# Optimization experiments

Hardware: AMD Instinct MI355X
Metric: run time of the kernel (lower is better)

The kernel has to match this reference:

```python
import jax, jax.numpy as jnp
import numpy as np

N = 100000      # nodes
E = 800000      # edges (avg degree 8)
F = 61          # num_node_features (embedding dim); node feat = F+3 = 64 with pos
D = 64          # hidden_dim
OUT = 32        # output_dim
TYPES = 100     # num_node_types
G = 64          # number of graphs in the batch (global_mean_pool segments)
L = 4           # num_layers per SE3Transformer (from transformer_config)


def _mk(k, shape):
    return jax.random.normal(k, shape, jnp.float32) * 0.1


def setup_inputs() -> dict:
    key = jax.random.key(0)
    ks = jax.random.split(key, 24)
    din = F + 3  # cat([pos, embedding(z)])
    inp = {
        "pos": jax.random.normal(ks[0], (N, 3), jnp.float32),
        "z": jax.random.randint(ks[1], (N,), 0, TYPES),
        "edge_index": jax.random.randint(ks[2], (2, E), 0, N),
        "batch": jnp.sort(jax.random.randint(ks[3], (N,), 0, G)),
        "emb": _mk(ks[4], (TYPES, F)),
        # transformer1: input proj din->D, then L message-passing layers at width D
        "t1_Win": _mk(ks[5], (din, D)),
        "t1_W1": _mk(ks[6], (L, 2 * D + 1, D)), "t1_b1": jnp.zeros((L, D), jnp.float32),
        "t1_W2": _mk(ks[7], (L, D, D)),        "t1_b2": jnp.zeros((L, D), jnp.float32),
        "t1_W3": _mk(ks[8], (L, 2 * D, D)),    "t1_b3": jnp.zeros((L, D), jnp.float32),
        # transformer2: input proj D->D, then L layers at width D
        "t2_Win": _mk(ks[9], (D, D)),
        "t2_W1": _mk(ks[10], (L, 2 * D + 1, D)), "t2_b1": jnp.zeros((L, D), jnp.float32),
        "t2_W2": _mk(ks[11], (L, D, D)),         "t2_b2": jnp.zeros((L, D), jnp.float32),
        "t2_W3": _mk(ks[12], (L, 2 * D, D)),     "t2_b3": jnp.zeros((L, D), jnp.float32),
        # final Linear(hidden_dim, output_dim)
        "Wlin": _mk(ks[13], (D, OUT)), "blin": jnp.zeros((OUT,), jnp.float32),
    }
    return inp


def _transformer(h, pos, src, dst, Win, W1, b1, W2, b2, W3, b3):
    """Equivariant graph transformer block: input projection + L distance-
    conditioned message-passing layers with residual updates."""
    h = h @ Win  # [N, D]
    # squared pairwise distance per edge -> rotation/translation invariant
    d2 = jnp.sum((pos[src] - pos[dst]) ** 2, axis=-1, keepdims=True)  # [E, 1]

    def layer(h, p):
        W1, b1, W2, b2, W3, b3 = p
        m = jnp.concatenate([h[src], h[dst], d2], axis=-1)        # [E, 2D+1]
        m = jax.nn.relu(m @ W1 + b1) @ W2 + b2                    # [E, D]
        agg = jax.ops.segment_sum(m, dst, num_segments=N)          # [N, D]
        h = h + jax.nn.relu(jnp.concatenate([h, agg], axis=-1) @ W3 + b3)
        return h, None

    h, _ = jax.lax.scan(layer, h, (W1, b1, W2, b2, W3, b3))
    return h


def reference(pos, z, edge_index, batch, emb,
              t1_Win, t1_W1, t1_b1, t1_W2, t1_b2, t1_W3, t1_b3,
              t2_Win, t2_W1, t2_b1, t2_W2, t2_b2, t2_W3, t2_b3,
              Wlin, blin):
    src, dst = edge_index[0], edge_index[1]
    x = jnp.concatenate([pos, emb[z]], axis=-1)  # [N, 3+F]
    x = jax.nn.relu(_transformer(x, pos, src, dst, t1_Win, t1_W1, t1_b1, t1_W2, t1_b2, t1_W3, t1_b3))
    x = jax.nn.relu(_transformer(x, pos, src, dst, t2_Win, t2_W1, t2_b1, t2_W2, t2_b2, t2_W3, t2_b3))
    x = x @ Wlin + blin  # [N, OUT]
    # global_mean_pool over graph ids
    counts = jax.ops.segment_sum(jnp.ones((N,), x.dtype), batch, num_segments=G)
    pooled = jax.ops.segment_sum(x, batch, num_segments=G) / jnp.clip(counts, 1.0)[:, None]
    return pooled  # [G, OUT]
```

## Files before the change

### kernel.cpp

```cpp
#include <hip/hip_runtime.h>
#include <hip/hip_bf16.h>

typedef unsigned short u16;
typedef unsigned int   u32;
typedef short bf16x8 __attribute__((ext_vector_type(8)));
typedef float f32x4  __attribute__((ext_vector_type(4)));

#define NN 100000
#define EE 800000
#define NTILE 6250
#define NTB   1563
#define EBLK  1792
#define TOTW  (EBLK * 4)
#define SCB   98
#define GMAX  (NN + EE / 8 + 2)

#define MFMA16(a,b,c) __builtin_amdgcn_mfma_f32_16x16x32_bf16(a,b,c,0,0,0)

__device__ __forceinline__ float b2f(u16 u) {
    u32 x = ((u32)u) << 16;
    return __uint_as_float(x);
}
__device__ __forceinline__ u16 f2b(float f) {
    __hip_bfloat16 h = __float2bfloat16(f);
    return *reinterpret_cast<u16*>(&h);
}
__device__ __forceinline__ void splt(float v, u16& hi, u16& lo) {
    hi = f2b(v);
    lo = f2b(v - b2f(hi));
}

__global__ __launch_bounds__(256) void k_deg(const int* __restrict__ dst,
                                             int* __restrict__ deg) {
    int e = blockIdx.x * 256 + threadIdx.x;
    if (e < EE) atomicAdd(&deg[dst[e]], 1);
}

__global__ __launch_bounds__(1024) void k_scanA(const int* __restrict__ deg,
                                                int* __restrict__ part) {
    __shared__ int s[1024];
    int i = blockIdx.x * 1024 + threadIdx.x;
    int v = (i < NN) ? deg[i] : 0;
    s[threadIdx.x] = v;
    __syncthreads();
    for (int off = 512; off > 0; off >>= 1) {
        if ((int)threadIdx.x < off) s[threadIdx.x] += s[threadIdx.x + off];
        __syncthreads();
    }
    if (threadIdx.x == 0) part[blockIdx.x] = s[0];
}

__global__ void k_scanB(int* __restrict__ part) {
    if (threadIdx.x == 0 && blockIdx.x == 0) {
        int run = 0;
        for (int b = 0; b < SCB; ++b) { int v = part[b]; part[b] = run; run += v; }
        part[SCB] = run;
    }
}

__global__ __launch_bounds__(1024) void k_scanC(const int* __restrict__ deg,
                                                const int* __restrict__ part,
                                                int* __restrict__ rowptr) {
    __shared__ int s[1024];
    int i = blockIdx.x * 1024 + threadIdx.x;
    int v = (i < NN) ? deg[i] : 0;
    s[threadIdx.x] = v;
    __syncthreads();
    for (int off = 1; off < 1024; off <<= 1) {
        int t = ((int)threadIdx.x >= off) ? s[threadIdx.x - off] : 0;
        __syncthreads();
        s[threadIdx.x] += t;
        __syncthreads();
    }
    int incl = s[threadIdx.x];
    if (i < NN) rowptr[i] = part[blockIdx.x] + incl - v;
    if (i == NN - 1) rowptr[NN] = part[SCB];
}

__global__ __launch_bounds__(256) void k_scatter(const int* __restrict__ src,
                                                 const int* __restrict__ dst,
                                                 const float* __restrict__ pos,
                                                 int* __restrict__ cursor,
                                                 int* __restrict__ srcc,
                                                 float* __restrict__ d2c) {
    int e = blockIdx.x * 256 + threadIdx.x;
    if (e >= EE) return;
    if (e < 16) { srcc[EE + e] = 0; d2c[EE + e] = 0.f; }
    int d = dst[e], s = src[e];
    int p = atomicAdd(&cursor[d], 1);
    srcc[p] = s;
    float dx = pos[s * 3 + 0] - pos[d * 3 + 0];
    float dy = pos[s * 3 + 1] - pos[d * 3 + 1];
    float dz = pos[s * 3 + 2] - pos[d * 3 + 2];
    d2c[p] = dx * dx + dy * dy + dz * dz;
}

__global__ __launch_bounds__(256) void k_ngrp(const int* __restrict__ deg,
                                              int* __restrict__ ngrp) {
    int i = blockIdx.x * 256 + threadIdx.x;
    if (i < NN) ngrp[i] = (deg[i] + 7) >> 3;
}

__global__ __launch_bounds__(256) void k_gfill(const int* __restrict__ deg,
                                               const int* __restrict__ rowptr,
                                               const int* __restrict__ grp_ptr,
                                               int* __restrict__ gnode,
                                               int* __restrict__ gstart,
                                               int* __restrict__ gcnt) {
    int n = blockIdx.x * 256 + threadIdx.x;
    if (n >= NN) return;
    int d = deg[n];
    int ng = (d + 7) >> 3;
    int base = grp_ptr[n], rp = rowptr[n];
    for (int k = 0; k < ng; ++k) {
        gnode[base + k] = n;
        gstart[base + k] = rp + 8 * k;
        int cc = d - 8 * k; if (cc > 8) cc = 8;
        gcnt[base + k] = cc;
    }
}

__global__ __launch_bounds__(256) void k_swz(const float* t1W1, const float* t1W2, const float* t1W3,
                                             const float* t2W1, const float* t2W2, const float* t2W3,
                                             const float* t1Win, const float* t2Win,
                                             u16* __restrict__ WsA, u16* __restrict__ WsB) {
    int gid = blockIdx.x * 256 + threadIdx.x;
    if (gid < 163840) {
        int L = gid / 20480;
        int r = gid % 20480;
        const float* W1 = (L < 4 ? t1W1 : t2W1) + (size_t)(L & 3) * 129 * 64;
        const float* W2 = (L < 4 ? t1W2 : t2W2) + (size_t)(L & 3) * 64 * 64;
        const float* W3 = (L < 4 ? t1W3 : t2W3) + (size_t)(L & 3) * 128 * 64;
        float w;
        int rr, f, e, lane, j, row, col;
        if (r < 8192) { rr = r; f = rr >> 9; e = rr & 511; lane = e >> 3; j = e & 7;
            row = (f >> 2) * 32 + (lane >> 4) * 8 + j; col = (f & 3) * 16 + (lane & 15);
            w = W1[row * 64 + col];
        } else if (r < 12288) { rr = r - 8192; f = rr >> 9; e = rr & 511; lane = e >> 3; j = e & 7;
            row = (f >> 2) * 32 + (lane >> 4) * 8 + j; col = (f & 3) * 16 + (lane & 15);
            w = W2[row * 64 + col];
        } else { rr = r - 12288; f = rr >> 9; e = rr & 511; lane = e >> 3; j = e & 7;
            row = (f >> 2) * 32 + (lane >> 4) * 8 + j; col = (f & 3) * 16 + (lane & 15);
            w = W3[row * 64 + col];
        }
        u16 hi, lo; splt(w, hi, lo);
        WsA[(size_t)L * 40960 + r] = hi;
        WsA[(size_t)L * 40960 + 20480 + r] = lo;
    } else {
        int t = gid - 163840;
        int sel = (t < 4096) ? 0 : 1;
        int rr = t & 4095;
        const float* Win = sel ? t2Win : t1Win;
        int f = rr >> 9, e = rr & 511, lane = e >> 3, j = e & 7;
        int row = (f >> 2) * 32 + (lane >> 4) * 8 + j;
        int col = (f & 3) * 16 + (lane & 15);
        float w = Win[row * 64 + col];
        u16 hi, lo; splt(w, hi, lo);
        WsB[sel * 8192 + rr] = hi;
        WsB[sel * 8192 + 4096 + rr] = lo;
    }
}

__global__ __launch_bounds__(256) void k_proj1(const float* __restrict__ pos,
                                               const int* __restrict__ z,
                                               const float* __restrict__ emb,
                                               const u16* __restrict__ WinS,
                                               u16* __restrict__ hbx) {
    int tile = blockIdx.x * 4 + (threadIdx.x >> 6);
    if (tile >= NTILE) return;
    int lane = threadIdx.x & 63, c = lane & 15, g = lane >> 4;
    int n0 = tile * 16, nr = n0 + c;
    int zr = z[nr];
    const float* er = emb + (long)zr * 61 - 3;
    bf16x8 A0h, A0l, A1h, A1l;
#pragma unroll
    for (int j = 0; j < 8; ++j) {
        int f = 8 * g + j;
        float v1 = (f < 3) ? pos[nr * 3 + (f < 3 ? f : 0)] : er[f];
        float v2 = er[32 + 8 * g + j];
        u16 hi, lo;
        splt(v1, hi, lo); A0h[j] = (short)hi; A0l[j] = (short)lo;
        splt(v2, hi, lo); A1h[j] = (short)hi; A1l[j] = (short)lo;
    }
    const bf16x8* Wh = (const bf16x8*)WinS;
    const bf16x8* Wl = (const bf16x8*)(WinS + 4096);
#pragma unroll
    for (int nt = 0; nt < 4; ++nt) {
        f32x4 acc = {0.f, 0.f, 0.f, 0.f};
        acc = MFMA16(A0h, Wh[nt * 64 + lane], acc);
        acc = MFMA16(A1h, Wh[(4 + nt) * 64 + lane], acc);
        acc = MFMA16(A0l, Wh[nt * 64 + lane], acc);
        acc = MFMA16(A1l, Wh[(4 + nt) * 64 + lane], acc);
        acc = MFMA16(A0h, Wl[nt * 64 + lane], acc);
        acc = MFMA16(A1h, Wl[(4 + nt) * 64 + lane], acc);
#pragma unroll
        for (int r = 0; r < 4; ++r) {
            long n = n0 + 4 * g + r;
            u16 hi, lo; splt(acc[r], hi, lo);
            hbx[n * 128 + nt * 16 + c] = hi;
            hbx[n * 128 + 64 + nt * 16 + c] = lo;
        }
    }
}

__global__ __launch_bounds__(256) void k_proj2(const u16* __restrict__ WinS,
                                               u16* __restrict__ hbx) {
    int tile = blockIdx.x * 4 + (threadIdx.x >> 6);
    if (tile >= NTILE) return;
    int lane = threadIdx.x & 63, c = lane & 15, g = lane >> 4;
    int n0 = tile * 16, nr = n0 + c;
    const bf16x8* p = (const bf16x8*)(hbx + (long)nr * 128);
    bf16x8 h0 = p[g], h1 = p[g + 4], l0 = p[g + 8], l1 = p[g + 12];
    bf16x8 A0h, A0l, A1h, A1l;
#pragma unroll
    for (int j = 0; j < 8; ++j) {
        float v1 = fmaxf(b2f((u16)h0[j]) + b2f((u16)l0[j]), 0.f);
        float v2 = fmaxf(b2f((u16)h1[j]) + b2f((u16)l1[j]), 0.f);
        u16 hi, lo;
        splt(v1, hi, lo); A0h[j] = (short)hi; A0l[j] = (short)lo;
        splt(v2, hi, lo); A1h[j] = (short)hi; A1l[j] = (short)lo;
    }
    const bf16x8* Wh = (const bf16x8*)WinS;
    const bf16x8* Wl = (const bf16x8*)(WinS + 4096);
#pragma unroll
    for (int nt = 0; nt < 4; ++nt) {
        f32x4 acc = {0.f, 0.f, 0.f, 0.f};
        acc = MFMA16(A0h, Wh[nt * 64 + lane], acc);
        acc = MFMA16(A1h, Wh[(4 + nt) * 64 + lane], acc);
        acc = MFMA16(A0l, Wh[nt * 64 + lane], acc);
        acc = MFMA16(A1l, Wh[(4 + nt) * 64 + lane], acc);
        acc = MFMA16(A0h, Wl[nt * 64 + lane], acc);
        acc = MFMA16(A1h, Wl[(4 + nt) * 64 + lane], acc);
#pragma unroll
        for (int r = 0; r < 4; ++r) {
            long n = n0 + 4 * g + r;
            u16 hi, lo; splt(acc[r], hi, lo);
            hbx[n * 128 + nt * 16 + c] = hi;
            hbx[n * 128 + 64 + nt * 16 + c] = lo;
        }
    }
}

__global__ __launch_bounds__(256) void k_dsthalf(const u16* __restrict__ hbx,
                                                 const u16* __restrict__ Wsl,
                                                 const float* __restrict__ b1,
                                                 float* __restrict__ accbT) {
    int tile = blockIdx.x * 4 + (threadIdx.x >> 6);
    if (tile >= NTILE) return;
    int lane = threadIdx.x & 63, c = lane & 15, g = lane >> 4;
    int n0 = tile * 16, nr = n0 + c;
    const bf16x8* W1h = (const bf16x8*)Wsl;
    const bf16x8* W1l = (const bf16x8*)(Wsl + 20480);
    const bf16x8* p = (const bf16x8*)(hbx + (long)nr * 128);
    bf16x8 A0h = p[g], A1h = p[g + 4], A0l = p[g + 8], A1l = p[g + 12];
    f32x4 acc4[4];
#pragma unroll
    for (int nt = 0; nt < 4; ++nt) {
        float bv = b1[nt * 16 + c];
        f32x4 acc = {bv, bv, bv, bv};
        acc = MFMA16(A0h, W1h[(8 + nt) * 64 + lane], acc);
        acc = MFMA16(A1h, W1h[(12 + nt) * 64 + lane], acc);
        acc = MFMA16(A0l, W1h[(8 + nt) * 64 + lane], acc);
        acc = MFMA16(A1l, W1h[(12 + nt) * 64 + lane], acc);
        acc = MFMA16(A0h, W1l[(8 + nt) * 64 + lane], acc);
        acc = MFMA16(A1h, W1l[(12 + nt) * 64 + lane], acc);
        acc4[nt] = acc;
    }
#pragma unroll
    for (int r = 0; r < 4; ++r) {
        f32x4 w = {acc4[0][r], acc4[1][r], acc4[2][r], acc4[3][r]};
        *(f32x4*)(accbT + (long)(n0 + 4 * g + r) * 64 + c * 4) = w;
    }
}

__global__ __launch_bounds__(256) void k_edges_mfma(const u16* __restrict__ hbx,
                                                    float* __restrict__ sgrp,
                                                    const float* __restrict__ d2c,
                                                    const int* __restrict__ srcc,
                                                    const int* __restrict__ gnode,
                                                    const int* __restrict__ gstart,
                                                    const int* __restrict__ gcnt,
                                                    const int* __restrict__ grp_ptr,
                                                    const u16* __restrict__ Wsl,
                                                    const float* __restrict__ W1f,
                                                    const float* __restrict__ accbT) {
    int lane = threadIdx.x & 63;
    int wid = blockIdx.x * 4 + (threadIdx.x >> 6);
    int c = lane & 15, g = lane >> 4;
    const bf16x8* W1H = (const bf16x8*)Wsl;
    const bf16x8* W1L = (const bf16x8*)(Wsl + 20480);
    bf16x8 w1h[2][4], w1l[2][4];
#pragma unroll
    for (int ks = 0; ks < 2; ++ks)
#pragma unroll
        for (int nt = 0; nt < 4; ++nt) {
            w1h[ks][nt] = W1H[(ks * 4 + nt) * 64 + lane];
            w1l[ks][nt] = W1L[(ks * 4 + nt) * 64 + lane];
        }
    float wdc[4];
#pragma unroll
    for (int nt = 0; nt < 4; ++nt) wdc[nt] = W1f[128 * 64 + nt * 16 + c];

    int G = grp_ptr[NN];
    int T = (G + 1) >> 1;

    for (int ti = wid; ti < T; ti += TOTW) {
        int ga = 2 * ti, gb = 2 * ti + 1;
        int na = gnode[ga], sa = gstart[ga], ca = gcnt[ga];
        int nb = na, sb = sa, cb = 0;
        if (gb < G) { nb = gnode[gb]; sb = gstart[gb]; cb = gcnt[gb]; }

        int nsel = (g < 2) ? na : nb;
        int ssel = (g < 2) ? sa : sb;
        int csel = (g < 2) ? ca : cb;
        int ro = 4 * (g & 1);

        f32x4 bse = *(const f32x4*)(accbT + (long)nsel * 64 + c * 4);

        int t = (c < 8) ? (sa + c) : (sb + c - 8);
        int s = srcc[t];
        const bf16x8* sp = (const bf16x8*)(hbx + (long)s * 128);
        bf16x8 A0h = sp[g], A1h = sp[g + 4], A0l = sp[g + 8], A1l = sp[g + 12];

        float dq[4];
#pragma unroll
        for (int r = 0; r < 4; ++r) dq[r] = d2c[ssel + ro + r];

        float sv[4];
#pragma unroll
        for (int nt = 0; nt < 4; ++nt) {
            f32x4 ci;
#pragma unroll
            for (int r = 0; r < 4; ++r) ci[r] = bse[nt] + dq[r] * wdc[nt];
            ci = MFMA16(A0h, w1h[0][nt], ci);
            ci = MFMA16(A1h, w1h[1][nt], ci);
            ci = MFMA16(A0l, w1h[0][nt], ci);
            ci = MFMA16(A1l, w1h[1][nt], ci);
            ci = MFMA16(A0h, w1l[0][nt], ci);
            ci = MFMA16(A1h, w1l[1][nt], ci);
            float s4 = 0.f;
#pragma unroll
            for (int r = 0; r < 4; ++r)
                s4 += (ro + r < csel) ? fmaxf(ci[r], 0.f) : 0.f;
            s4 += __shfl_xor(s4, 16);
            sv[nt] = s4;
        }
        if (g == 0) {
#pragma unroll
            for (int nt = 0; nt < 4; ++nt)
                sgrp[(long)ga * 64 + nt * 16 + c] = sv[nt];
        }
        if (g == 2 && gb < G) {
#pragma unroll
            for (int nt = 0; nt < 4; ++nt)
                sgrp[(long)gb * 64 + nt * 16 + c] = sv[nt];
        }
    }
}

__global__ __launch_bounds__(256) void k_node2(u16* __restrict__ hbx,
                                               const float* __restrict__ sgrp,
                                               const int* __restrict__ grp_ptr,
                                               const int* __restrict__ deg,
                                               const u16* __restrict__ Wsl,
                                               const float* __restrict__ b2,
                                               const float* __restrict__ b3,
                                               const u16* __restrict__ WslN,
                                               const float* __restrict__ b1N,
                                               float* __restrict__ accbT) {
    __shared__ u16 th[4][16 * 72];
    __shared__ u16 tl[4][16 * 72];
    int w = threadIdx.x >> 6, lane = threadIdx.x & 63;
    int tile = blockIdx.x * 4 + w;
    if (tile >= NTILE) return;
    int c = lane & 15, g = lane >> 4;
    int n0 = tile * 16, nr = n0 + c;
    u16* lh = th[w];
    u16* ll = tl[w];

    const bf16x8* W2H = (const bf16x8*)(Wsl + 8192);
    const bf16x8* W2L = (const bf16x8*)(Wsl + 28672);
    const bf16x8* W3H = (const bf16x8*)(Wsl + 12288);
    const bf16x8* W3L = (const bf16x8*)(Wsl + 32768);

    int gp0 = grp_ptr[nr], gp1 = grp_ptr[nr + 1];
    f32x4 sA0 = {0, 0, 0, 0}, sA1 = {0, 0, 0, 0};
    f32x4 sB0 = {0, 0, 0, 0}, sB1 = {0, 0, 0, 0};
    for (int gi = gp0; gi < gp1; ++gi) {
        const f32x4* q = (const f32x4*)(sgrp + (long)gi * 64 + 8 * g);
        const f32x4* q2 = (const f32x4*)(sgrp + (long)gi * 64 + 32 + 8 * g);
        sA0 += q[0]; sA1 += q[1];
        sB0 += q2[0]; sB1 += q2[1];
    }
    bf16x8 S0h, S0l, S1h, S1l;
#pragma unroll
    for (int j = 0; j < 4; ++j) {
        u16 hi, lo;
        splt(sA0[j], hi, lo); S0h[j] = (short)hi; S0l[j] = (short)lo;
        splt(sA1[j], hi, lo); S0h[4 + j] = (short)hi; S0l[4 + j] = (short)lo;
        splt(sB0[j], hi, lo); S1h[j] = (short)hi; S1l[j] = (short)lo;
        splt(sB1[j], hi, lo); S1h[4 + j] = (short)hi; S1l[4 + j] = (short)lo;
    }

    const bf16x8* hp = (const bf16x8*)(hbx + (long)nr * 128);
    bf16x8 H0h = hp[g], H1h = hp[g + 4], H0l = hp[g + 8], H1l = hp[g + 12];

    float dg[4];
#pragma unroll
    for (int r = 0; r < 4; ++r) dg[r] = (float)deg[n0 + 4 * g + r];

#pragma unroll
    for (int nt = 0; nt < 4; ++nt) {
        float b2c = b2[nt * 16 + c];
        f32x4 a = {dg[0] * b2c, dg[1] * b2c, dg[2] * b2c, dg[3] * b2c};
        a = MFMA16(S0h, W2H[nt * 64 + lane], a);
        a = MFMA16(S1h, W2H[(4 + nt) * 64 + lane], a);
        a = MFMA16(S0l, W2H[nt * 64 + lane], a);
        a = MFMA16(S1l, W2H[(4 + nt) * 64 + lane], a);
        a = MFMA16(S0h, W2L[nt * 64 + lane], a);
        a = MFMA16(S1h, W2L[(4 + nt) * 64 + lane], a);
#pragma unroll
        for (int r = 0; r < 4; ++r) {
            u16 hi, lo; splt(a[r], hi, lo);
            lh[(4 * g + r) * 72 + nt * 16 + c] = hi;
            ll[(4 * g + r) * 72 + nt * 16 + c] = lo;
        }
    }
    bf16x8 G0h = *(const bf16x8*)(lh + c * 72 + g * 8);
    bf16x8 G1h = *(const bf16x8*)(lh + c * 72 + 32 + g * 8);
    bf16x8 G0l = *(const bf16x8*)(ll + c * 72 + g * 8);
    bf16x8 G1l = *(const bf16x8*)(ll + c * 72 + 32 + g * 8);

    f32x4 u4[4];
#pragma unroll
    for (int nt = 0; nt < 4; ++nt) {
        float bv = b3[nt * 16 + c];
        f32x4 u = {bv, bv, bv, bv};
        u = MFMA16(H0h, W3H[nt * 64 + lane], u);
        u = MFMA16(H1h, W3H[(4 + nt) * 64 + lane], u);
        u = MFMA16(G0h, W3H[(8 + nt) * 64 + lane], u);
        u = MFMA16(G1h, W3H[(12 + nt) * 64 + lane], u);
        u = MFMA16(H0l, W3H[nt * 64 + lane], u);
        u = MFMA16(H1l, W3H[(4 + nt) * 64 + lane], u);
        u = MFMA16(G0l, W3H[(8 + nt) * 64 + lane], u);
        u = MFMA16(G1l, W3H[(12 + nt) * 64 + lane], u);
        u = MFMA16(H0h, W3L[nt * 64 + lane], u);
        u = MFMA16(H1h, W3L[(4 + nt) * 64 + lane], u);
        u = MFMA16(G0h, W3L[(8 + nt) * 64 + lane], u);
        u = MFMA16(G1h, W3L[(12 + nt) * 64 + lane], u);
        u4[nt] = u;
    }

#pragma unroll
    for (int nt = 0; nt < 4; ++nt)
#pragma unroll
        for (int r = 0; r < 4; ++r) {
            long n = n0 + 4 * g + r;
            long ix = n * 128 + nt * 16 + c;
            float ho = b2f(hbx[ix]) + b2f(hbx[ix + 64]);
            float hn = ho + fmaxf(u4[nt][r], 0.f);
            u16 hi, lo; splt(hn, hi, lo);
            hbx[ix] = hi;
            hbx[ix + 64] = lo;
            lh[(4 * g + r) * 72 + nt * 16 + c] = hi;
            ll[(4 * g + r) * 72 + nt * 16 + c] = lo;
        }

    if (WslN) {
        bf16x8 N0h = *(const bf16x8*)(lh + c * 72 + g * 8);
        bf16x8 N1h = *(const bf16x8*)(lh + c * 72 + 32 + g * 8);
        bf16x8 N0l = *(const bf16x8*)(ll + c * 72 + g * 8);
        bf16x8 N1l = *(const bf16x8*)(ll + c * 72 + 32 + g * 8);
        const bf16x8* W1h = (const bf16x8*)WslN;
        const bf16x8* W1l = (const bf16x8*)(WslN + 20480);
        f32x4 acc4[4];
#pragma unroll
        for (int nt = 0; nt < 4; ++nt) {
            float bv = b1N[nt * 16 + c];
            f32x4 a = {bv, bv, bv, bv};
            a = MFMA16(N0h, W1h[(8 + nt) * 64 + lane], a);
            a = MFMA16(N1h, W1h[(12 + nt) * 64 + lane], a);
            a = MFMA16(N0l, W1h[(8 + nt) * 64 + lane], a);
            a = MFMA16(N1l, W1h[(12 + nt) * 64 + lane], a);
            a = MFMA16(N0h, W1l[(8 + nt) * 64 + lane], a);
            a = MFMA16(N1h, W1l[(12 + nt) * 64 + lane], a);
            acc4[nt] = a;
        }
#pragma unroll
        for (int r = 0; r < 4; ++r) {
            f32x4 wv = {acc4[0][r], acc4[1][r], acc4[2][r], acc4[3][r]};
            *(f32x4*)(accbT + (long)(n0 + 4 * g + r) * 64 + c * 4) = wv;
        }
    }
}

__global__ void k_granges(const int* __restrict__ batch, int* __restrict__ gpt) {
    int g = blockIdx.x * blockDim.x + threadIdx.x;
    if (g > 64) return;
    int lo = 0, hi = NN;
    while (lo < hi) {
        int mid = (lo + hi) >> 1;
        if (batch[mid] < g) lo = mid + 1; else hi = mid;
    }
    gpt[g] = lo;
}

__global__ __launch_bounds__(256) void k_sumrelu(const u16* __restrict__ hbx,
                                                 const int* __restrict__ gpt,
                                                 float* __restrict__ sumh) {
    int g = blockIdx.x >> 3, sp = blockIdx.x & 7;
    int lo = gpt[g], hi = gpt[g + 1];
    int n = hi - lo;
    int per = (n + 7) / 8;
    int s0 = lo + sp * per;
    int s1 = s0 + per; if (s1 > hi) s1 = hi;
    int lane = threadIdx.x & 63, wv = threadIdx.x >> 6;
    float acc = 0.f;
    for (int i = s0 + wv; i < s1; i += 4) {
        float v = b2f(hbx[(long)i * 128 + lane]) + b2f(hbx[(long)i * 128 + 64 + lane]);
        acc += fmaxf(v, 0.f);
    }
    if (acc != 0.f || wv == 0)
        atomicAdd(&sumh[g * 64 + lane], acc);
}

__global__ __launch_bounds__(256) void k_outgemm(const float* __restrict__ sumh,
                                                 const int* __restrict__ gpt,
                                                 const float* __restrict__ Wlin,
                                                 const float* __restrict__ blin,
                                                 float* __restrict__ out) {
    int idx = blockIdx.x * 256 + threadIdx.x;
    if (idx >= 64 * 32) return;
    int g = idx >> 5, o = idx & 31;
    int cnt = gpt[g + 1] - gpt[g];
    float acc = 0.f;
#pragma unroll 8
    for (int k = 0; k < 64; ++k)
        acc += sumh[g * 64 + k] * Wlin[k * 32 + o];
    out[idx] = (cnt > 0) ? (acc / (float)cnt + blin[o]) : 0.f;
}

extern "C" void kernel_launch(void* const* d_in, const int* in_sizes, int n_in,
                              void* d_out, int out_size, void* d_ws, size_t ws_size,
                              hipStream_t stream) {
    const float* pos    = (const float*)d_in[0];
    const int*   z      = (const int*)d_in[1];
    const int*   ei     = (const int*)d_in[2];
    const int*   batch  = (const int*)d_in[3];
    const float* emb    = (const float*)d_in[4];
    const float* t1_Win = (const float*)d_in[5];
    const float* t1_W1  = (const float*)d_in[6];
    const float* t1_b1  = (const float*)d_in[7];
    const float* t1_W2  = (const float*)d_in[8];
    const float* t1_b2  = (const float*)d_in[9];
    const float* t1_W3  = (const float*)d_in[10];
    const float* t1_b3  = (const float*)d_in[11];
    const float* t2_Win = (const float*)d_in[12];
    const float* t2_W1  = (const float*)d_in[13];
    const float* t2_b1  = (const float*)d_in[14];
    const float* t2_W2  = (const float*)d_in[15];
    const float* t2_b2  = (const float*)d_in[16];
    const float* t2_W3  = (const float*)d_in[17];
    const float* t2_b3  = (const float*)d_in[18];
    const float* Wlin   = (const float*)d_in[19];
    const float* blin   = (const float*)d_in[20];

    const int* srcI = ei;
    const int* dstI = ei + EE;

    char* ws = (char*)d_ws;
    size_t off = 0;
    auto alloc = [&](size_t bytes) -> void* {
        void* p = ws + off;
        off += (bytes + 255) / 256 * 256;
        return p;
    };
    float* accbT   = (float*)alloc((size_t)NN * 64 * 4);
    u16*   hbx     = (u16*)alloc((size_t)NN * 128 * 2);
    float* sgrp    = (float*)alloc((size_t)GMAX * 64 * 4);
    int*   rowptr  = (int*)alloc((size_t)(NN + 1) * 4);
    int*   deg     = (int*)alloc((size_t)NN * 4);
    int*   cursor  = (int*)alloc((size_t)NN * 4);
    int*   ngrpA   = (int*)alloc((size_t)NN * 4);
    int*   grp_ptr = (int*)alloc((size_t)(NN + 1) * 4);
    int*   gnode   = (int*)alloc((size_t)GMAX * 4);
    int*   gstart  = (int*)alloc((size_t)GMAX * 4);
    int*   gcnt    = (int*)alloc((size_t)GMAX * 4);
    int*   srcc    = (int*)alloc((size_t)(EE + 16) * 4);
    float* d2c     = (float*)alloc((size_t)(EE + 16) * 4);
    int*   gpt     = (int*)alloc(65 * 4);
    float* sumh    = (float*)alloc(64 * 64 * 4);
    int*   part    = (int*)alloc((SCB + 1) * 4);
    u16*   WsA     = (u16*)alloc((size_t)8 * 40960 * 2);
    u16*   WsB     = (u16*)alloc((size_t)16384 * 2);

    hipMemsetAsync(deg, 0, (size_t)NN * 4, stream);
    k_deg<<<(EE + 255) / 256, 256, 0, stream>>>(dstI, deg);
    k_scanA<<<SCB, 1024, 0, stream>>>(deg, part);
    k_scanB<<<1, 64, 0, stream>>>(part);
    k_scanC<<<SCB, 1024, 0, stream>>>(deg, part, rowptr);
    hipMemcpyAsync(cursor, rowptr, (size_t)NN * 4, hipMemcpyDeviceToDevice, stream);
    k_scatter<<<(EE + 255) / 256, 256, 0, stream>>>(srcI, dstI, pos, cursor, srcc, d2c);
    k_ngrp<<<(NN + 255) / 256, 256, 0, stream>>>(deg, ngrpA);
    k_scanA<<<SCB, 1024, 0, stream>>>(ngrpA, part);
    k_scanB<<<1, 64, 0, stream>>>(part);
    k_scanC<<<SCB, 1024, 0, stream>>>(ngrpA, part, grp_ptr);
    k_gfill<<<(NN + 255) / 256, 256, 0, stream>>>(deg, rowptr, grp_ptr, gnode, gstart, gcnt);
    k_swz<<<172032 / 256, 256, 0, stream>>>(t1_W1, t1_W2, t1_W3, t2_W1, t2_W2, t2_W3,
                                            t1_Win, t2_Win, WsA, WsB);
    k_granges<<<1, 128, 0, stream>>>(batch, gpt);

    k_proj1<<<NTB, 256, 0, stream>>>(pos, z, emb, WsB, hbx);
    k_dsthalf<<<NTB, 256, 0, stream>>>(hbx, WsA, t1_b1, accbT);
    for (int l = 0; l < 4; ++l) {
        const u16* Wsl = WsA + (size_t)l * 40960;
        k_edges_mfma<<<EBLK, 256, 0, stream>>>(hbx, sgrp, d2c, srcc, gnode, gstart,
                                               gcnt, grp_ptr, Wsl,
                                               t1_W1 + (size_t)l * 129 * 64, accbT);
        const u16* WslN = (l < 3) ? (WsA + (size_t)(l + 1) * 40960) : nullptr;
        const float* b1N = (l < 3) ? (t1_b1 + (size_t)(l + 1) * 64) : nullptr;
        k_node2<<<NTB, 256, 0, stream>>>(hbx, sgrp, grp_ptr, deg, Wsl,
                                         t1_b2 + (size_t)l * 64, t1_b3 + (size_t)l * 64,
                                         WslN, b1N, accbT);
    }

    k_proj2<<<NTB, 256, 0, stream>>>(WsB + 8192, hbx);
    k_dsthalf<<<NTB, 256, 0, stream>>>(hbx, WsA + (size_t)4 * 40960, t2_b1, accbT);
    for (int l = 0; l < 4; ++l) {
        const u16* Wsl = WsA + (size_t)(4 + l) * 40960;
        k_edges_mfma<<<EBLK, 256, 0, stream>>>(hbx, sgrp, d2c, srcc, gnode, gstart,
                                               gcnt, grp_ptr, Wsl,
                                               t2_W1 + (size_t)l * 129 * 64, accbT);
        const u16* WslN = (l < 3) ? (WsA + (size_t)(5 + l) * 40960) : nullptr;
        const float* b1N = (l < 3) ? (t2_b1 + (size_t)(l + 1) * 64) : nullptr;
        k_node2<<<NTB, 256, 0, stream>>>(hbx, sgrp, grp_ptr, deg, Wsl,
                                         t2_b2 + (size_t)l * 64, t2_b3 + (size_t)l * 64,
                                         WslN, b1N, accbT);
    }

    hipMemsetAsync(sumh, 0, 64 * 64 * 4, stream);
    k_sumrelu<<<64 * 8, 256, 0, stream>>>(hbx, gpt, sumh);
    k_outgemm<<<8, 256, 0, stream>>>(sumh, gpt, Wlin, blin, (float*)d_out);
}
```

Before: 1.057 ms.

## Scatter edges into padded 8-slot group layout and pack group table

The edge scatter now writes source indices and squared distances directly into group-padded slots of 8 per group. The edge kernel can then load its 16 source ids and its distances with contiguous vector loads instead of going through gstart indirection. The three group arrays (node, start, count) are packed into one int per group, loaded as an int2 per tile. The edge grid is also reduced from 1792 to 1536 blocks. The cost is three extra memsets and padded arrays, with padded slots zero-filled so they point to node 0.

Measured after the change: 907.7 us. -14.1%, faster.

```diff
diff --git a/kernel.cpp b/kernel.cpp
--- a/kernel.cpp
+++ b/kernel.cpp
@@ -5,12 +5,13 @@
 typedef unsigned int   u32;
 typedef short bf16x8 __attribute__((ext_vector_type(8)));
 typedef float f32x4  __attribute__((ext_vector_type(4)));
+typedef int   i32x2  __attribute__((ext_vector_type(2)));
 
 #define NN 100000
 #define EE 800000
 #define NTILE 6250
 #define NTB   1563
-#define EBLK  1792
+#define EBLK  1536
 #define TOTW  (EBLK * 4)
 #define SCB   98
 #define GMAX  (NN + EE / 8 + 2)
@@ -80,19 +81,22 @@
 __global__ __launch_bounds__(256) void k_scatter(const int* __restrict__ src,
                                                  const int* __restrict__ dst,
                                                  const float* __restrict__ pos,
+                                                 const int* __restrict__ rowptr,
+                                                 const int* __restrict__ grp_ptr,
                                                  int* __restrict__ cursor,
-                                                 int* __restrict__ srcc,
-                                                 float* __restrict__ d2c) {
+                                                 int* __restrict__ srcg,
+                                                 float* __restrict__ d2g) {
     int e = blockIdx.x * 256 + threadIdx.x;
     if (e >= EE) return;
-    if (e < 16) { srcc[EE + e] = 0; d2c[EE + e] = 0.f; }
     int d = dst[e], s = src[e];
     int p = atomicAdd(&cursor[d], 1);
-    srcc[p] = s;
+    int off = p - rowptr[d];
+    long slot = (long)(grp_ptr[d] + (off >> 3)) * 8 + (off & 7);
+    srcg[slot] = s;
     float dx = pos[s * 3 + 0] - pos[d * 3 + 0];
     float dy = pos[s * 3 + 1] - pos[d * 3 + 1];
     float dz = pos[s * 3 + 2] - pos[d * 3 + 2];
-    d2c[p] = dx * dx + dy * dy + dz * dz;
+    d2g[slot] = dx * dx + dy * dy + dz * dz;
 }
 
 __global__ __launch_bounds__(256) void k_ngrp(const int* __restrict__ deg,
@@ -101,22 +105,17 @@
     if (i < NN) ngrp[i] = (deg[i] + 7) >> 3;
 }
 
-__global__ __launch_bounds__(256) void k_gfill(const int* __restrict__ deg,
-                                               const int* __restrict__ rowptr,
-                                               const int* __restrict__ grp_ptr,
-                                               int* __restrict__ gnode,
-                                               int* __restrict__ gstart,
-                                               int* __restrict__ gcnt) {
+__global__ __launch_bounds__(256) void k_gtab(const int* __restrict__ deg,
+                                              const int* __restrict__ grp_ptr,
+                                              int* __restrict__ gtab) {
     int n = blockIdx.x * 256 + threadIdx.x;
     if (n >= NN) return;
     int d = deg[n];
     int ng = (d + 7) >> 3;
-    int base = grp_ptr[n], rp = rowptr[n];
+    int base = grp_ptr[n];
     for (int k = 0; k < ng; ++k) {
-        gnode[base + k] = n;
-        gstart[base + k] = rp + 8 * k;
         int cc = d - 8 * k; if (cc > 8) cc = 8;
-        gcnt[base + k] = cc;
+        gtab[base + k] = (n << 4) | cc;
     }
 }
 
@@ -275,11 +274,9 @@
 
 __global__ __launch_bounds__(256) void k_edges_mfma(const u16* __restrict__ hbx,
                                                     float* __restrict__ sgrp,
-                                                    const float* __restrict__ d2c,
-                                                    const int* __restrict__ srcc,
-                                                    const int* __restrict__ gnode,
-                                                    const int* __restrict__ gstart,
-                                                    const int* __restrict__ gcnt,
+                                                    const float* __restrict__ d2g,
+                                                    const int* __restrict__ srcg,
+                                                    const int* __restrict__ gtab,
                                                     const int* __restrict__ grp_ptr,
                                                     const u16* __restrict__ Wsl,
                                                     const float* __restrict__ W1f,
@@ -303,28 +300,19 @@
 
     int G = grp_ptr[NN];
     int T = (G + 1) >> 1;
+    int ro = 4 * (g & 1);
 
     for (int ti = wid; ti < T; ti += TOTW) {
-        int ga = 2 * ti, gb = 2 * ti + 1;
-        int na = gnode[ga], sa = gstart[ga], ca = gcnt[ga];
-        int nb = na, sb = sa, cb = 0;
-        if (gb < G) { nb = gnode[gb]; sb = gstart[gb]; cb = gcnt[gb]; }
-
-        int nsel = (g < 2) ? na : nb;
-        int ssel = (g < 2) ? sa : sb;
-        int csel = (g < 2) ? ca : cb;
-        int ro = 4 * (g & 1);
+        i32x2 pk = *(const i32x2*)(gtab + 2 * ti);
+        int psel = (g < 2) ? pk[0] : pk[1];
+        int nsel = psel >> 4;
+        int csel = psel & 15;
 
         f32x4 bse = *(const f32x4*)(accbT + (long)nsel * 64 + c * 4);
-
-        int t = (c < 8) ? (sa + c) : (sb + c - 8);
-        int s = srcc[t];
+        int s = srcg[(long)ti * 16 + c];
         const bf16x8* sp = (const bf16x8*)(hbx + (long)s * 128);
         bf16x8 A0h = sp[g], A1h = sp[g + 4], A0l = sp[g + 8], A1l = sp[g + 12];
-
-        float dq[4];
-#pragma unroll
-        for (int r = 0; r < 4; ++r) dq[r] = d2c[ssel + ro + r];
+        f32x4 dq = *(const f32x4*)(d2g + (long)ti * 16 + 8 * (g >> 1) + ro);
 
         float sv[4];
 #pragma unroll
@@ -348,12 +336,12 @@
         if (g == 0) {
 #pragma unroll
             for (int nt = 0; nt < 4; ++nt)
-                sgrp[(long)ga * 64 + nt * 16 + c] = sv[nt];
-        }
-        if (g == 2 && gb < G) {
+                sgrp[(long)(2 * ti) * 64 + nt * 16 + c] = sv[nt];
+        }
+        if (g == 2 && 2 * ti + 1 < G) {
 #pragma unroll
             for (int nt = 0; nt < 4; ++nt)
-                sgrp[(long)gb * 64 + nt * 16 + c] = sv[nt];
+                sgrp[(long)(2 * ti + 1) * 64 + nt * 16 + c] = sv[nt];
         }
     }
 }
@@ -583,11 +571,9 @@
     int*   cursor  = (int*)alloc((size_t)NN * 4);
     int*   ngrpA   = (int*)alloc((size_t)NN * 4);
     int*   grp_ptr = (int*)alloc((size_t)(NN + 1) * 4);
-    int*   gnode   = (int*)alloc((size_t)GMAX * 4);
-    int*   gstart  = (int*)alloc((size_t)GMAX * 4);
-    int*   gcnt    = (int*)alloc((size_t)GMAX * 4);
-    int*   srcc    = (int*)alloc((size_t)(EE + 16) * 4);
-    float* d2c     = (float*)alloc((size_t)(EE + 16) * 4);
+    int*   gtab    = (int*)alloc((size_t)(GMAX + 2) * 4);
+    int*   srcg    = (int*)alloc((size_t)GMAX * 8 * 4);
+    float* d2g     = (float*)alloc((size_t)GMAX * 8 * 4);
     int*   gpt     = (int*)alloc(65 * 4);
     float* sumh    = (float*)alloc(64 * 64 * 4);
     int*   part    = (int*)alloc((SCB + 1) * 4);
@@ -595,17 +581,21 @@
     u16*   WsB     = (u16*)alloc((size_t)16384 * 2);
 
     hipMemsetAsync(deg, 0, (size_t)NN * 4, stream);
+    hipMemsetAsync(srcg, 0, (size_t)GMAX * 8 * 4, stream);
+    hipMemsetAsync(d2g, 0, (size_t)GMAX * 8 * 4, stream);
+    hipMemsetAsync(gtab, 0, (size_t)(GMAX + 2) * 4, stream);
     k_deg<<<(EE + 255) / 256, 256, 0, stream>>>(dstI, deg);
     k_scanA<<<SCB, 1024, 0, stream>>>(deg, part);
     k_scanB<<<1, 64, 0, stream>>>(part);
     k_scanC<<<SCB, 1024, 0, stream>>>(deg, part, rowptr);
-    hipMemcpyAsync(cursor, rowptr, (size_t)NN * 4, hipMemcpyDeviceToDevice, stream);
-    k_scatter<<<(EE + 255) / 256, 256, 0, stream>>>(srcI, dstI, pos, cursor, srcc, d2c);
     k_ngrp<<<(NN + 255) / 256, 256, 0, stream>>>(deg, ngrpA);
     k_scanA<<<SCB, 1024, 0, stream>>>(ngrpA, part);
     k_scanB<<<1, 64, 0, stream>>>(part);
     k_scanC<<<SCB, 1024, 0, stream>>>(ngrpA, part, grp_ptr);
-    k_gfill<<<(NN + 255) / 256, 256, 0, stream>>>(deg, rowptr, grp_ptr, gnode, gstart, gcnt);
+    hipMemcpyAsync(cursor, rowptr, (size_t)NN * 4, hipMemcpyDeviceToDevice, stream);
+    k_scatter<<<(EE + 255) / 256, 256, 0, stream>>>(srcI, dstI, pos, rowptr, grp_ptr,
+                                                    cursor, srcg, d2g);
+    k_gtab<<<(NN + 255) / 256, 256, 0, stream>>>(deg, grp_ptr, gtab);
     k_swz<<<172032 / 256, 256, 0, stream>>>(t1_W1, t1_W2, t1_W3, t2_W1, t2_W2, t2_W3,
                                             t1_Win, t2_Win, WsA, WsB);
     k_granges<<<1, 128, 0, stream>>>(batch, gpt);
@@ -614,9 +604,8 @@
     k_dsthalf<<<NTB, 256, 0, stream>>>(hbx, WsA, t1_b1, accbT);
     for (int l = 0; l < 4; ++l) {
         const u16* Wsl = WsA + (size_t)l * 40960;
-        k_edges_mfma<<<EBLK, 256, 0, stream>>>(hbx, sgrp, d2c, srcc, gnode, gstart,
-                                               gcnt, grp_ptr, Wsl,
-                                               t1_W1 + (size_t)l * 129 * 64, accbT);
+        k_edges_mfma<<<EBLK, 256, 0, stream>>>(hbx, sgrp, d2g, srcg, gtab, grp_ptr,
+                                               Wsl, t1_W1 + (size_t)l * 129 * 64, accbT);
         const u16* WslN = (l < 3) ? (WsA + (size_t)(l + 1) * 40960) : nullptr;
         const float* b1N = (l < 3) ? (t1_b1 + (size_t)(l + 1) * 64) : nullptr;
         k_node2<<<NTB, 256, 0, stream>>>(hbx, sgrp, grp_ptr, deg, Wsl,
@@ -628,9 +617,8 @@
     k_dsthalf<<<NTB, 256, 0, stream>>>(hbx, WsA + (size_t)4 * 40960, t2_b1, accbT);
     for (int l = 0; l < 4; ++l) {
         const u16* Wsl = WsA + (size_t)(4 + l) * 40960;
-        k_edges_mfma<<<EBLK, 256, 0, stream>>>(hbx, sgrp, d2c, srcc, gnode, gstart,
-                                               gcnt, grp_ptr, Wsl,
-                                               t2_W1 + (size_t)l * 129 * 64, accbT);
+        k_edges_mfma<<<EBLK, 256, 0, stream>>>(hbx, sgrp, d2g, srcg, gtab, grp_ptr,
+                                               Wsl, t2_W1 + (size_t)l * 129 * 64, accbT);
         const u16* WslN = (l < 3) ? (WsA + (size_t)(5 + l) * 40960) : nullptr;
         const float* b1N = (l < 3) ? (t2_b1 + (size_t)(l + 1) * 64) : nullptr;
         k_node2<<<NTB, 256, 0, stream>>>(hbx, sgrp, grp_ptr, deg, Wsl,
```
